# Kernel optimization log

Hardware: AMD Instinct MI355X
Metric: run time of the kernel (lower is better)

The kernel has to match this reference:

```python
import jax, jax.numpy as jnp
import numpy as np

HIDDEN = 1024
HEADS = 16
D_K = HIDDEN // HEADS
NEG_INF = -jnp.inf


def setup_inputs() -> dict:
    key = jax.random.key(0)
    ks = jax.random.split(key, 9)
    N, S = 4, 2048
    scale = 1.0 / np.sqrt(HIDDEN)
    x = jax.random.normal(ks[0], (N, S, HIDDEN), dtype=jnp.float32)
    attn_mask = jnp.ones((N, S), dtype=jnp.int32)
    Wq = jax.random.normal(ks[1], (HIDDEN, HIDDEN), dtype=jnp.float32) * scale
    bq = jnp.zeros((HIDDEN,), dtype=jnp.float32)
    Wk = jax.random.normal(ks[2], (HIDDEN, HIDDEN), dtype=jnp.float32) * scale
    bk = jnp.zeros((HIDDEN,), dtype=jnp.float32)
    Wv = jax.random.normal(ks[3], (HIDDEN, HIDDEN), dtype=jnp.float32) * scale
    bv = jnp.zeros((HIDDEN,), dtype=jnp.float32)
    Wp = jax.random.normal(ks[4], (HIDDEN, HIDDEN), dtype=jnp.float32) * scale
    bp = jnp.zeros((HIDDEN,), dtype=jnp.float32)
    return {"x": x, "attn_mask": attn_mask, "Wq": Wq, "bq": bq,
            "Wk": Wk, "bk": bk, "Wv": Wv, "bv": bv, "Wp": Wp, "bp": bp}


def reference(x, attn_mask, Wq, bq, Wk, bk, Wv, bv, Wp, bp):
    N, S, _ = x.shape
    H, dk = HEADS, D_K
    # torch nn.Linear: y = x @ W.T + b
    q = (x @ Wq.T + bq).reshape(N, S, H, dk).transpose(0, 2, 1, 3)  # (N,H,S,dk)
    k = (x @ Wk.T + bk).reshape(N, S, H, dk).transpose(0, 2, 1, 3)
    v = (x @ Wv.T + bv).reshape(N, S, H, dk).transpose(0, 2, 1, 3)
    attn = jnp.einsum('nhqd,nhkd->nhqk', q, k) / jnp.sqrt(jnp.float32(dk))
    mask = attn_mask.reshape(N, 1, 1, S)
    attn = jnp.where(mask == 0, NEG_INF, attn)
    attn = jax.nn.softmax(attn, axis=-1)
    # dropout is identity in eval mode
    y = jnp.einsum('nhqk,nhkd->nhqd', attn, v)  # (N,H,S,dk)
    y = y.transpose(0, 2, 1, 3).reshape(N, S, H * dk)
    return y @ Wp.T + bp
```

## Files before the change

### kernel.cpp

```cpp
#include <hip/hip_runtime.h>

typedef unsigned short u16;
typedef unsigned int u32;
typedef unsigned long long u64;
typedef __attribute__((ext_vector_type(8))) short bf16x8;
typedef __attribute__((ext_vector_type(4))) short bf16x4;
typedef __attribute__((ext_vector_type(4))) float f32x4;
typedef __attribute__((ext_vector_type(2))) unsigned int u32x2;

#define AS1(p) ((const __attribute__((address_space(1))) void*)(p))
#define AS3(p) ((__attribute__((address_space(3))) void*)(p))

__device__ __forceinline__ u16 f2bf(float f) {
    u32 u = __float_as_uint(f);
    u += 0x7fff + ((u >> 16) & 1);
    return (u16)(u >> 16);
}
__device__ __forceinline__ u32 pack2bf(float lo, float hi) {
    u32 a = __float_as_uint(lo) + 0x8000u;
    u32 b = __float_as_uint(hi) + 0x8000u;
    return __builtin_amdgcn_perm(b, a, 0x07060302);
}
__device__ __forceinline__ u32 cvtpk(float lo, float hi) {
    u32 r;
    asm("v_cvt_pk_bf16_f32 %0, %1, %2" : "=v"(r) : "v"(lo), "v"(hi));
    return r;
}

__device__ __forceinline__ void async16(const u16* g, u16* l) {
    __builtin_amdgcn_global_load_lds(AS1(g), AS3(l), 16, 0, 0);
}

__global__ __launch_bounds__(256) void cvt_kernel(const float* __restrict__ src,
                                                  u16* __restrict__ dst, int n) {
    int idx = (blockIdx.x * 256 + threadIdx.x) * 8;
    if (idx >= n) return;
    float4 a = *(const float4*)(src + idx);
    float4 b = *(const float4*)(src + idx + 4);
    uint4 o;
    o.x = (u32)f2bf(a.x) | ((u32)f2bf(a.y) << 16);
    o.y = (u32)f2bf(a.z) | ((u32)f2bf(a.w) << 16);
    o.z = (u32)f2bf(b.x) | ((u32)f2bf(b.y) << 16);
    o.w = (u32)f2bf(b.z) | ((u32)f2bf(b.w) << 16);
    *(uint4*)(dst + idx) = o;
}

__global__ __launch_bounds__(256) void cvt4_kernel(
    const float* __restrict__ s0, const float* __restrict__ s1,
    const float* __restrict__ s2, const float* __restrict__ s3,
    u16* __restrict__ d0, u16* __restrict__ d1,
    u16* __restrict__ d2, u16* __restrict__ d3) {
    const float* s; u16* d;
    switch (blockIdx.y) {
        case 0:  s = s0; d = d0; break;
        case 1:  s = s1; d = d1; break;
        case 2:  s = s2; d = d2; break;
        default: s = s3; d = d3; break;
    }
    int idx = (blockIdx.x * 256 + threadIdx.x) * 8;
    float4 a = *(const float4*)(s + idx);
    float4 b = *(const float4*)(s + idx + 4);
    uint4 o;
    o.x = (u32)f2bf(a.x) | ((u32)f2bf(a.y) << 16);
    o.y = (u32)f2bf(a.z) | ((u32)f2bf(a.w) << 16);
    o.z = (u32)f2bf(b.x) | ((u32)f2bf(b.y) << 16);
    o.w = (u32)f2bf(b.z) | ((u32)f2bf(b.w) << 16);
    *(uint4*)(d + idx) = o;
}

__global__ __launch_bounds__(256, 2) void gemm_bt(
    const u16* __restrict__ A,
    const u16* __restrict__ Wa, const u16* __restrict__ Wb, const u16* __restrict__ Wc,
    const float* __restrict__ ba, const float* __restrict__ bb, const float* __restrict__ bc,
    void* oa, void* ob_, void* oc, int mode)
{
    constexpr int K = 1024;
    __shared__ u16 smem[128 * 132];
    u16* At = smem;
    u16* Wt = smem + 4096;

    const int tid = threadIdx.x;
    const int lane = tid & 63, wv = tid >> 6;
    const int l15 = lane & 15, quad = lane >> 4;
    const int wr = wv >> 1, wc = wv & 1;

    const int L = blockIdx.x + (blockIdx.y << 3) + (blockIdx.z << 9);
    const int g = L & 7;
    const int j = L >> 3;
    const int z = j >> 6;
    const int r = j & 63;
    const int m0 = ((g << 3) + (r & 7)) * 128;
    const int n0 = (r >> 3) * 128;

    const u16* W = (z == 0) ? Wa : ((z == 1) ? Wb : Wc);
    const float* bs = (z == 0) ? ba : ((z == 1) ? bb : bc);
    void* out = (z == 0) ? oa : ((z == 1) ? ob_ : oc);
    const bool swap_ = (mode == 1) || (z < 2);

    f32x4 acc[4][4];
#pragma unroll
    for (int i = 0; i < 4; ++i)
#pragma unroll
        for (int j2 = 0; j2 < 4; ++j2) acc[i][j2] = (f32x4)0.f;

    const int call0 = wv * 2;
    for (int kk = 0; kk < K; kk += 32) {
#pragma unroll
        for (int jj = 0; jj < 2; ++jj) {
            int c = (call0 + jj) * 64 + lane;
            int row = c >> 2;
            int ko = ((c & 3) ^ (row & 3)) * 8;
            async16(A + (size_t)(m0 + row) * K + kk + ko, &At[(call0 + jj) * 512 + lane * 8]);
            async16(W + (size_t)(n0 + row) * K + kk + ko, &Wt[(call0 + jj) * 512 + lane * 8]);
        }
        __syncthreads();

        bf16x8 af[4], wf[4];
#pragma unroll
        for (int t = 0; t < 4; ++t) {
            int rowa = wr * 64 + t * 16 + l15;
            af[t] = *(const bf16x8*)&At[rowa * 32 + ((quad ^ (rowa & 3)) * 8)];
            int rowb = wc * 64 + t * 16 + l15;
            wf[t] = *(const bf16x8*)&Wt[rowb * 32 + ((quad ^ (rowb & 3)) * 8)];
        }
        if (swap_) {
#pragma unroll
            for (int rt = 0; rt < 4; ++rt)
#pragma unroll
                for (int ct = 0; ct < 4; ++ct)
                    acc[rt][ct] = __builtin_amdgcn_mfma_f32_16x16x32_bf16(wf[ct], af[rt], acc[rt][ct], 0, 0, 0);
        } else {
#pragma unroll
            for (int rt = 0; rt < 4; ++rt)
#pragma unroll
                for (int ct = 0; ct < 4; ++ct)
                    acc[rt][ct] = __builtin_amdgcn_mfma_f32_16x16x32_bf16(af[rt], wf[ct], acc[rt][ct], 0, 0, 0);
        }
        __syncthreads();
    }

    if (mode == 1) {
#pragma unroll
        for (int rt = 0; rt < 4; ++rt)
#pragma unroll
            for (int ct = 0; ct < 4; ++ct) {
                int m_ = m0 + wr * 64 + rt * 16 + l15;
                int ob = n0 + wc * 64 + ct * 16 + quad * 4;
                float4 b4 = *(const float4*)&bs[ob];
                float4 v;
                v.x = acc[rt][ct][0] + b4.x;
                v.y = acc[rt][ct][1] + b4.y;
                v.z = acc[rt][ct][2] + b4.z;
                v.w = acc[rt][ct][3] + b4.w;
                *(float4*)((float*)out + (size_t)m_ * 1024 + ob) = v;
            }
        return;
    }

    const int n = m0 >> 11, s0 = m0 & 2047;
    if (z < 2) {
        const float qs = (z == 0) ? 0.18033688011112042f : 1.0f;
#pragma unroll
        for (int rt = 0; rt < 4; ++rt)
#pragma unroll
            for (int ct = 0; ct < 4; ++ct) {
                int ml = wr * 64 + rt * 16 + l15;
                int ol = wc * 64 + ct * 16 + quad * 4;
                float4 b4 = *(const float4*)&bs[n0 + ol];
                float v0 = (acc[rt][ct][0] + b4.x) * qs;
                float v1 = (acc[rt][ct][1] + b4.y) * qs;
                float v2 = (acc[rt][ct][2] + b4.z) * qs;
                float v3 = (acc[rt][ct][3] + b4.w) * qs;
                u32x2 pv = { pack2bf(v0, v1), pack2bf(v2, v3) };
                *(u32x2*)&smem[ml * 132 + ol] = pv;
            }
        __syncthreads();
        const int h0 = n0 >> 6;
#pragma unroll
        for (int p = 0; p < 8; ++p) {
            int hh = p >> 2, qq = p & 3;
            int m = qq * 32 + (tid >> 3), d = (tid & 7) * 8;
            bf16x8 vv = *(const bf16x8*)&smem[m * 132 + hh * 64 + d];
            u16* dst = (u16*)out + ((size_t)((n * 16 + h0 + hh) * 2048 + s0 + m)) * 64 + d;
            *(bf16x8*)dst = vv;
        }
    } else {
#pragma unroll
        for (int rt = 0; rt < 4; ++rt)
#pragma unroll
            for (int ct = 0; ct < 4; ++ct) {
                int ol = wc * 64 + ct * 16 + l15;
                int ml = wr * 64 + rt * 16 + quad * 4;
                float b = bs[n0 + ol];
                float v0 = acc[rt][ct][0] + b;
                float v1 = acc[rt][ct][1] + b;
                float v2 = acc[rt][ct][2] + b;
                float v3 = acc[rt][ct][3] + b;
                u32x2 pv = { pack2bf(v0, v1), pack2bf(v2, v3) };
                *(u32x2*)&smem[ol * 132 + ml] = pv;
            }
        __syncthreads();
#pragma unroll
        for (int p = 0; p < 8; ++p) {
            int o = p * 16 + (tid >> 4), ms = (tid & 15) * 8;
            bf16x8 vv = *(const bf16x8*)&smem[o * 132 + ms];
            int og = n0 + o;
            int h = og >> 6, d = og & 63;
            u16* dst = (u16*)out + ((size_t)((n * 16 + h) * 64 + d)) * 2048 + s0 + ms;
            *(bf16x8*)dst = vv;
        }
    }
}

__global__ __launch_bounds__(256, 2) void attn_kernel(
    const u16* __restrict__ Q, const u16* __restrict__ K_,
    const u16* __restrict__ VT, const int* __restrict__ mask,
    u16* __restrict__ Y)
{
    constexpr int S = 2048, DK = 64, STR = 72;
    __shared__ u16 Kt[2][64 * STR];
    __shared__ u16 Vt[2][64 * STR];

    const int tid = threadIdx.x;
    const int lane = tid & 63, w = tid >> 6;
    const int l15 = lane & 15, quad = lane >> 4;

    const int L = blockIdx.x + (blockIdx.y << 3);
    const int vb = (L & 7) * 64 + (L >> 3);
    const int nh = vb >> 3;
    const int n = nh >> 4, h = nh & 15;
    const int qbase = (vb & 7) * 256;

    const u16* Qh = Q + (size_t)nh * S * DK;
    const u16* Kh = K_ + (size_t)nh * S * DK;
    const u16* Vh = VT + (size_t)nh * DK * S;

    bf16x8 qf[4][2];
#pragma unroll
    for (int nt = 0; nt < 4; ++nt)
#pragma unroll
        for (int st = 0; st < 2; ++st)
            qf[nt][st] = *(const bf16x8*)(Qh + (size_t)(qbase + w * 64 + nt * 16 + l15) * DK + st * 32 + quad * 8);

    f32x4 o[4][4];
#pragma unroll
    for (int dt = 0; dt < 4; ++dt)
#pragma unroll
        for (int nt = 0; nt < 4; ++nt) o[dt][nt] = (f32x4)0.f;
    float lsum[4] = {0.f, 0.f, 0.f, 0.f};

    const int r0 = tid >> 3, c8 = (tid & 7) * 8;

    u32 bm = 0;
    for (int t = 0; t < 32; ++t) {
        int mv = mask[n * S + t * 64 + lane];
        if (__ballot(mv != 0) == ~0ull) bm |= (1u << t);
    }

    {
        bf16x8 k0 = *(const bf16x8*)(Kh + (size_t)r0 * 64 + c8);
        bf16x8 k1 = *(const bf16x8*)(Kh + (size_t)(r0 + 32) * 64 + c8);
        bf16x8 v0 = *(const bf16x8*)(Vh + (size_t)r0 * S + c8);
        bf16x8 v1 = *(const bf16x8*)(Vh + (size_t)(r0 + 32) * S + c8);
        *(bf16x8*)&Kt[0][r0 * STR + c8] = k0;
        *(bf16x8*)&Kt[0][(r0 + 32) * STR + c8] = k1;
        *(bf16x8*)&Vt[0][r0 * STR + c8] = v0;
        *(bf16x8*)&Vt[0][(r0 + 32) * STR + c8] = v1;
    }
    __syncthreads();

    const f32x4 zf = (f32x4)0.f;

    for (int it = 0; it < 32; ++it) {
        const int cur = it & 1, nxt = cur ^ 1;
        const u16* Ktc = &Kt[cur][0];
        const u16* Vtc = &Vt[cur][0];

        const int kkn = ((it + 1) << 6) & (S - 1);
        bf16x8 rk0 = *(const bf16x8*)(Kh + (size_t)(kkn + r0) * 64 + c8);
        bf16x8 rk1 = *(const bf16x8*)(Kh + (size_t)(kkn + r0 + 32) * 64 + c8);
        bf16x8 rv0 = *(const bf16x8*)(Vh + (size_t)r0 * S + kkn + c8);
        bf16x8 rv1 = *(const bf16x8*)(Vh + (size_t)(r0 + 32) * S + kkn + c8);

        f32x4 sacc[4][4];
        __builtin_amdgcn_s_setprio(1);
#pragma unroll
        for (int jt = 0; jt < 4; ++jt) {
            bf16x8 kf = *(const bf16x8*)&Ktc[(jt * 16 + l15) * STR + quad * 8];
#pragma unroll
            for (int nt = 0; nt < 4; ++nt)
                sacc[jt][nt] = __builtin_amdgcn_mfma_f32_16x16x32_bf16(kf, qf[nt][0], zf, 0, 0, 0);
        }
#pragma unroll
        for (int jt = 0; jt < 4; ++jt) {
            bf16x8 kf = *(const bf16x8*)&Ktc[(jt * 16 + l15) * STR + 32 + quad * 8];
#pragma unroll
            for (int nt = 0; nt < 4; ++nt)
                sacc[jt][nt] = __builtin_amdgcn_mfma_f32_16x16x32_bf16(kf, qf[nt][1], sacc[jt][nt], 0, 0, 0);
        }
        __builtin_amdgcn_s_setprio(0);

        if (!((bm >> it) & 1)) {
#pragma unroll
            for (int jt = 0; jt < 4; ++jt)
#pragma unroll
                for (int r = 0; r < 4; ++r) {
                    int mv = mask[n * S + it * 64 + jt * 16 + quad * 4 + r];
#pragma unroll
                    for (int nt = 0; nt < 4; ++nt)
                        if (mv == 0) sacc[jt][nt][r] = -1e30f;
                }
        }

        bf16x8 pb[4][2];
#pragma unroll
        for (int nt = 0; nt < 4; ++nt) {
            float ps = 0.f;
            u32 pkx[4], pky[4];
#pragma unroll
            for (int jt = 0; jt < 4; ++jt) {
                float e0 = __builtin_amdgcn_exp2f(sacc[jt][nt][0]);
                float e1 = __builtin_amdgcn_exp2f(sacc[jt][nt][1]);
                float e2 = __builtin_amdgcn_exp2f(sacc[jt][nt][2]);
                float e3 = __builtin_amdgcn_exp2f(sacc[jt][nt][3]);
                ps += (e0 + e1) + (e2 + e3);
                pkx[jt] = cvtpk(e0, e1);
                pky[jt] = cvtpk(e2, e3);
            }
            lsum[nt] += ps;
#pragma unroll
            for (int kt = 0; kt < 2; ++kt) {
                auto rX = __builtin_amdgcn_permlane32_swap(pkx[2 * kt], pkx[2 * kt + 1], false, false);
                auto rY = __builtin_amdgcn_permlane32_swap(pky[2 * kt], pky[2 * kt + 1], false, false);
                auto sX = __builtin_amdgcn_permlane16_swap(rX[0], rX[1], false, false);
                auto sY = __builtin_amdgcn_permlane16_swap(rY[0], rY[1], false, false);
                union { u32 u[4]; bf16x8 v; } pu;
                pu.u[0] = sX[0];
                pu.u[1] = sY[0];
                pu.u[2] = sX[1];
                pu.u[3] = sY[1];
                pb[nt][kt] = pu.v;
            }
        }

        *(bf16x8*)&Kt[nxt][r0 * STR + c8] = rk0;
        *(bf16x8*)&Kt[nxt][(r0 + 32) * STR + c8] = rk1;
        *(bf16x8*)&Vt[nxt][r0 * STR + c8] = rv0;
        *(bf16x8*)&Vt[nxt][(r0 + 32) * STR + c8] = rv1;

        __builtin_amdgcn_s_setprio(1);
#pragma unroll
        for (int kt = 0; kt < 2; ++kt) {
#pragma unroll
            for (int dt = 0; dt < 4; ++dt) {
                bf16x8 vf = *(const bf16x8*)&Vtc[(dt * 16 + l15) * STR + kt * 32 + quad * 8];
#pragma unroll
                for (int nt = 0; nt < 4; ++nt)
                    o[dt][nt] = __builtin_amdgcn_mfma_f32_16x16x32_bf16(vf, pb[nt][kt], o[dt][nt], 0, 0, 0);
            }
        }
        __builtin_amdgcn_s_setprio(0);

        __syncthreads();
    }

#pragma unroll
    for (int nt = 0; nt < 4; ++nt) {
        float ls = lsum[nt];
        ls += __shfl_xor(ls, 16);
        ls += __shfl_xor(ls, 32);
        float rl = (ls > 0.f) ? 1.f / ls : 0.f;
        int qi = qbase + w * 64 + nt * 16 + l15;
#pragma unroll
        for (int dt = 0; dt < 4; ++dt) {
            u32x2 pv = { pack2bf(o[dt][nt][0] * rl, o[dt][nt][1] * rl),
                         pack2bf(o[dt][nt][2] * rl, o[dt][nt][3] * rl) };
            size_t base = ((size_t)(n * 2048 + qi)) * 1024 + h * 64 + dt * 16 + quad * 4;
            *(u32x2*)(Y + base) = pv;
        }
    }
}

extern "C" void kernel_launch(void* const* d_in, const int* in_sizes, int n_in,
                              void* d_out, int out_size, void* d_ws, size_t ws_size,
                              hipStream_t stream) {
    const float* x  = (const float*)d_in[0];
    const int* mask = (const int*)d_in[1];
    const float* Wq = (const float*)d_in[2];
    const float* bq = (const float*)d_in[3];
    const float* Wk = (const float*)d_in[4];
    const float* bk = (const float*)d_in[5];
    const float* Wv = (const float*)d_in[6];
    const float* bv = (const float*)d_in[7];
    const float* Wp = (const float*)d_in[8];
    const float* bp = (const float*)d_in[9];

    char* ws = (char*)d_ws;
    u16* xb  = (u16*)(ws);
    u16* wqb = (u16*)(ws + (16u << 20));
    u16* wkb = (u16*)(ws + (18u << 20));
    u16* wvb = (u16*)(ws + (20u << 20));
    u16* wpb = (u16*)(ws + (22u << 20));
    u16* Qb  = (u16*)(ws + (24u << 20));
    u16* Kb  = (u16*)(ws + (40u << 20));
    u16* Vb  = (u16*)(ws + (56u << 20));
    u16* Yb  = (u16*)(ws + (72u << 20));

    cvt_kernel<<<4096, 256, 0, stream>>>(x, xb, 8388608);
    cvt4_kernel<<<dim3(512, 4), 256, 0, stream>>>(Wq, Wk, Wv, Wp, wqb, wkb, wvb, wpb);

    gemm_bt<<<dim3(8, 64, 3), 256, 0, stream>>>(xb, wqb, wkb, wvb, bq, bk, bv,
                                                (void*)Qb, (void*)Kb, (void*)Vb, 0);

    attn_kernel<<<dim3(8, 64), 256, 0, stream>>>(Qb, Kb, Vb, mask, Yb);

    gemm_bt<<<dim3(8, 64, 1), 256, 0, stream>>>(Yb, wpb, wpb, wpb, bp, bp, bp,
                                                d_out, d_out, d_out, 1);
}
```

Before: 277.1 us.

## Software-pipeline attention loop so QK^T of next tile overlaps softmax/PV of previous

Restructures the flash-attention inner loop so that the QK^T MFMAs for tile t are interleaved with the exp2/pack softmax work of tile t-1, using two ping-pong score register sets (X/Yc) and a manually unrolled-by-two macro body. The prologue now preloads two K/V tiles and computes the first score tile up front. This is meant to hide transcendental and permlane latency behind matrix-core work. In exchange it raises register pressure, adds a second barrier per iteration and makes the tail handling (last body wraps around via the modulo index) more intricate.

```diff
diff --git a/kernel.cpp b/kernel.cpp
--- a/kernel.cpp
+++ b/kernel.cpp
@@ -257,112 +257,117 @@
         if (__ballot(mv != 0) == ~0ull) bm |= (1u << t);
     }
 
-    {
-        bf16x8 k0 = *(const bf16x8*)(Kh + (size_t)r0 * 64 + c8);
-        bf16x8 k1 = *(const bf16x8*)(Kh + (size_t)(r0 + 32) * 64 + c8);
-        bf16x8 v0 = *(const bf16x8*)(Vh + (size_t)r0 * S + c8);
-        bf16x8 v1 = *(const bf16x8*)(Vh + (size_t)(r0 + 32) * S + c8);
-        *(bf16x8*)&Kt[0][r0 * STR + c8] = k0;
-        *(bf16x8*)&Kt[0][(r0 + 32) * STR + c8] = k1;
-        *(bf16x8*)&Vt[0][r0 * STR + c8] = v0;
-        *(bf16x8*)&Vt[0][(r0 + 32) * STR + c8] = v1;
+#pragma unroll
+    for (int t = 0; t < 2; ++t) {
+        bf16x8 k0 = *(const bf16x8*)(Kh + (size_t)(t * 64 + r0) * 64 + c8);
+        bf16x8 k1 = *(const bf16x8*)(Kh + (size_t)(t * 64 + r0 + 32) * 64 + c8);
+        bf16x8 v0 = *(const bf16x8*)(Vh + (size_t)r0 * S + t * 64 + c8);
+        bf16x8 v1 = *(const bf16x8*)(Vh + (size_t)(r0 + 32) * S + t * 64 + c8);
+        *(bf16x8*)&Kt[t][r0 * STR + c8] = k0;
+        *(bf16x8*)&Kt[t][(r0 + 32) * STR + c8] = k1;
+        *(bf16x8*)&Vt[t][r0 * STR + c8] = v0;
+        *(bf16x8*)&Vt[t][(r0 + 32) * STR + c8] = v1;
     }
     __syncthreads();
 
     const f32x4 zf = (f32x4)0.f;
-
-    for (int it = 0; it < 32; ++it) {
-        const int cur = it & 1, nxt = cur ^ 1;
-        const u16* Ktc = &Kt[cur][0];
-        const u16* Vtc = &Vt[cur][0];
-
-        const int kkn = ((it + 1) << 6) & (S - 1);
-        bf16x8 rk0 = *(const bf16x8*)(Kh + (size_t)(kkn + r0) * 64 + c8);
-        bf16x8 rk1 = *(const bf16x8*)(Kh + (size_t)(kkn + r0 + 32) * 64 + c8);
-        bf16x8 rv0 = *(const bf16x8*)(Vh + (size_t)r0 * S + kkn + c8);
-        bf16x8 rv1 = *(const bf16x8*)(Vh + (size_t)(r0 + 32) * S + kkn + c8);
-
-        f32x4 sacc[4][4];
-        __builtin_amdgcn_s_setprio(1);
-#pragma unroll
-        for (int jt = 0; jt < 4; ++jt) {
-            bf16x8 kf = *(const bf16x8*)&Ktc[(jt * 16 + l15) * STR + quad * 8];
-#pragma unroll
-            for (int nt = 0; nt < 4; ++nt)
-                sacc[jt][nt] = __builtin_amdgcn_mfma_f32_16x16x32_bf16(kf, qf[nt][0], zf, 0, 0, 0);
-        }
-#pragma unroll
-        for (int jt = 0; jt < 4; ++jt) {
-            bf16x8 kf = *(const bf16x8*)&Ktc[(jt * 16 + l15) * STR + 32 + quad * 8];
-#pragma unroll
-            for (int nt = 0; nt < 4; ++nt)
-                sacc[jt][nt] = __builtin_amdgcn_mfma_f32_16x16x32_bf16(kf, qf[nt][1], sacc[jt][nt], 0, 0, 0);
-        }
-        __builtin_amdgcn_s_setprio(0);
-
-        if (!((bm >> it) & 1)) {
-#pragma unroll
-            for (int jt = 0; jt < 4; ++jt)
-#pragma unroll
-                for (int r = 0; r < 4; ++r) {
-                    int mv = mask[n * S + it * 64 + jt * 16 + quad * 4 + r];
-#pragma unroll
-                    for (int nt = 0; nt < 4; ++nt)
-                        if (mv == 0) sacc[jt][nt][r] = -1e30f;
-                }
-        }
-
-        bf16x8 pb[4][2];
+    f32x4 X[4][4], Yc[4][4];
+
+    __builtin_amdgcn_s_setprio(1);
+#pragma unroll
+    for (int jt = 0; jt < 4; ++jt) {
+        bf16x8 kf0 = *(const bf16x8*)&Kt[0][(jt * 16 + l15) * STR + quad * 8];
+        bf16x8 kf1 = *(const bf16x8*)&Kt[0][(jt * 16 + l15) * STR + 32 + quad * 8];
 #pragma unroll
         for (int nt = 0; nt < 4; ++nt) {
-            float ps = 0.f;
-            u32 pkx[4], pky[4];
-#pragma unroll
-            for (int jt = 0; jt < 4; ++jt) {
-                float e0 = __builtin_amdgcn_exp2f(sacc[jt][nt][0]);
-                float e1 = __builtin_amdgcn_exp2f(sacc[jt][nt][1]);
-                float e2 = __builtin_amdgcn_exp2f(sacc[jt][nt][2]);
-                float e3 = __builtin_amdgcn_exp2f(sacc[jt][nt][3]);
-                ps += (e0 + e1) + (e2 + e3);
-                pkx[jt] = cvtpk(e0, e1);
-                pky[jt] = cvtpk(e2, e3);
-            }
-            lsum[nt] += ps;
-#pragma unroll
-            for (int kt = 0; kt < 2; ++kt) {
-                auto rX = __builtin_amdgcn_permlane32_swap(pkx[2 * kt], pkx[2 * kt + 1], false, false);
-                auto rY = __builtin_amdgcn_permlane32_swap(pky[2 * kt], pky[2 * kt + 1], false, false);
-                auto sX = __builtin_amdgcn_permlane16_swap(rX[0], rX[1], false, false);
-                auto sY = __builtin_amdgcn_permlane16_swap(rY[0], rY[1], false, false);
-                union { u32 u[4]; bf16x8 v; } pu;
-                pu.u[0] = sX[0];
-                pu.u[1] = sY[0];
-                pu.u[2] = sX[1];
-                pu.u[3] = sY[1];
-                pb[nt][kt] = pu.v;
-            }
-        }
-
-        *(bf16x8*)&Kt[nxt][r0 * STR + c8] = rk0;
-        *(bf16x8*)&Kt[nxt][(r0 + 32) * STR + c8] = rk1;
-        *(bf16x8*)&Vt[nxt][r0 * STR + c8] = rv0;
-        *(bf16x8*)&Vt[nxt][(r0 + 32) * STR + c8] = rv1;
-
-        __builtin_amdgcn_s_setprio(1);
-#pragma unroll
-        for (int kt = 0; kt < 2; ++kt) {
-#pragma unroll
-            for (int dt = 0; dt < 4; ++dt) {
-                bf16x8 vf = *(const bf16x8*)&Vtc[(dt * 16 + l15) * STR + kt * 32 + quad * 8];
-#pragma unroll
-                for (int nt = 0; nt < 4; ++nt)
-                    o[dt][nt] = __builtin_amdgcn_mfma_f32_16x16x32_bf16(vf, pb[nt][kt], o[dt][nt], 0, 0, 0);
-            }
-        }
-        __builtin_amdgcn_s_setprio(0);
-
-        __syncthreads();
-    }
+            X[jt][nt] = __builtin_amdgcn_mfma_f32_16x16x32_bf16(kf0, qf[nt][0], zf, 0, 0, 0);
+            X[jt][nt] = __builtin_amdgcn_mfma_f32_16x16x32_bf16(kf1, qf[nt][1], X[jt][nt], 0, 0, 0);
+        }
+    }
+    __builtin_amdgcn_s_setprio(0);
+
+#define BODY(SP, SC, ITC) do {                                                           \
+    const int cur_ = (ITC) & 1, prv_ = cur_ ^ 1;                                         \
+    const int tm_ = (ITC) - 1;                                                           \
+    const int kkn_ = (((ITC) + 1) << 6) & (S - 1);                                       \
+    bf16x8 rk0_ = *(const bf16x8*)(Kh + (size_t)(kkn_ + r0) * 64 + c8);                  \
+    bf16x8 rk1_ = *(const bf16x8*)(Kh + (size_t)(kkn_ + r0 + 32) * 64 + c8);             \
+    if (!((bm >> tm_) & 1)) {                            \
+        for (int jt = 0; jt < 4; ++jt)                                                   \
+            for (int rr = 0; rr < 4; ++rr) {                                             \
+                int mv = mask[n * S + tm_ * 64 + jt * 16 + quad * 4 + rr];               \
+                for (int nt = 0; nt < 4; ++nt)                                           \
+                    if (mv == 0) SP[jt][nt][rr] = -1e30f;                                \
+            }                                                                            \
+    }                                                                                    \
+    u32 pkx_[4][4], pky_[4][4];                                            \
+    float ps_[4] = {0.f, 0.f, 0.f, 0.f};                                                 \
+    __builtin_amdgcn_s_setprio(1);                                                       \
+    _Pragma("unroll")                                                                    \
+    for (int jt = 0; jt < 4; ++jt) {                                                     \
+        bf16x8 kf0 = *(const bf16x8*)&Kt[cur_][(jt * 16 + l15) * STR + quad * 8];        \
+        bf16x8 kf1 = *(const bf16x8*)&Kt[cur_][(jt * 16 + l15) * STR + 32 + quad * 8];   \
+        _Pragma("unroll")                                                                \
+        for (int nt = 0; nt < 4; ++nt) {                                                 \
+            SC[jt][nt] = __builtin_amdgcn_mfma_f32_16x16x32_bf16(kf0, qf[nt][0], zf, 0, 0, 0); \
+            SC[jt][nt] = __builtin_amdgcn_mfma_f32_16x16x32_bf16(kf1, qf[nt][1], SC[jt][nt], 0, 0, 0); \
+        }                                                                                \
+        _Pragma("unroll")                                                                \
+        for (int nt = 0; nt < 4; ++nt) {          \
+            float e0 = __builtin_amdgcn_exp2f(SP[jt][nt][0]);                            \
+            float e1 = __builtin_amdgcn_exp2f(SP[jt][nt][1]);                            \
+            float e2 = __builtin_amdgcn_exp2f(SP[jt][nt][2]);                            \
+            float e3 = __builtin_amdgcn_exp2f(SP[jt][nt][3]);                            \
+            ps_[nt] += (e0 + e1) + (e2 + e3);                                            \
+            pkx_[nt][jt] = cvtpk(e0, e1);                                                \
+            pky_[nt][jt] = cvtpk(e2, e3);                                                \
+        }                                                                                \
+    }                                                                                    \
+    __builtin_amdgcn_s_setprio(0);                                                       \
+    bf16x8 pb_[4][2];                                                                    \
+    _Pragma("unroll")                                                                    \
+    for (int nt = 0; nt < 4; ++nt) {                                                     \
+        lsum[nt] += ps_[nt];                                                             \
+        _Pragma("unroll")                                                                \
+        for (int kt = 0; kt < 2; ++kt) {                                                 \
+            auto rX_ = __builtin_amdgcn_permlane32_swap(pkx_[nt][2 * kt], pkx_[nt][2 * kt + 1], false, false); \
+            auto rY_ = __builtin_amdgcn_permlane32_swap(pky_[nt][2 * kt], pky_[nt][2 * kt + 1], false, false); \
+            auto sX_ = __builtin_amdgcn_permlane16_swap(rX_[0], rX_[1], false, false);   \
+            auto sY_ = __builtin_amdgcn_permlane16_swap(rY_[0], rY_[1], false, false);   \
+            union { u32 u[4]; bf16x8 v; } pu_;                                           \
+            pu_.u[0] = sX_[0]; pu_.u[1] = sY_[0]; pu_.u[2] = sX_[1]; pu_.u[3] = sY_[1];  \
+            pb_[nt][kt] = pu_.v;                                                         \
+        }                                                                                \
+    }                                                                                    \
+    bf16x8 rv0_ = *(const bf16x8*)(Vh + (size_t)r0 * S + kkn_ + c8);                     \
+    bf16x8 rv1_ = *(const bf16x8*)(Vh + (size_t)(r0 + 32) * S + kkn_ + c8);              \
+    __builtin_amdgcn_s_setprio(1);                                                       \
+    _Pragma("unroll")                                                                    \
+    for (int kt = 0; kt < 2; ++kt) {                                                     \
+        _Pragma("unroll")                                                                \
+        for (int dt = 0; dt < 4; ++dt) {                                                 \
+            bf16x8 vf_ = *(const bf16x8*)&Vt[prv_][(dt * 16 + l15) * STR + kt * 32 + quad * 8]; \
+            _Pragma("unroll")                                                            \
+            for (int nt = 0; nt < 4; ++nt)                                               \
+                o[dt][nt] = __builtin_amdgcn_mfma_f32_16x16x32_bf16(vf_, pb_[nt][kt], o[dt][nt], 0, 0, 0); \
+        }                                                                                \
+    }                                                                                    \
+    __builtin_amdgcn_s_setprio(0);                                                       \
+    __syncthreads();        \
+    *(bf16x8*)&Kt[prv_][r0 * STR + c8] = rk0_;                                           \
+    *(bf16x8*)&Kt[prv_][(r0 + 32) * STR + c8] = rk1_;                                    \
+    *(bf16x8*)&Vt[prv_][r0 * STR + c8] = rv0_;                                           \
+    *(bf16x8*)&Vt[prv_][(r0 + 32) * STR + c8] = rv1_;                                    \
+    __syncthreads();                                             \
+} while (0)
+
+    for (int b = 1; b < 31; b += 2) {
+        BODY(X, Yc, b);
+        BODY(Yc, X, b + 1);
+    }
+    BODY(X, Yc, 31);
+    BODY(Yc, X, 32);
+#undef BODY
 
 #pragma unroll
     for (int nt = 0; nt < 4; ++nt) {
```

Result: slower. 427.8 us (+54.4%).

## Double-buffer GEMM LDS tiles to overlap async global loads with MFMA

Applied to the files above, without the earlier changes.

Splits the shared-memory staging area of the projection GEMM into two buffers, so the async global-to-LDS loads for the next K-slice are issued while MFMAs run on the current slice. Each step now needs one barrier instead of two, and the source and destination addresses are precomputed outside the loop. Nothing new is allocated, since the existing 128x132 shared array already covers both buffers. The risks are a race if the waitcnt and barrier placement is wrong (waitcnt only covers the issuing thread's loads), and added register pressure under the 2-blocks-per-CU launch bound.

```diff
diff --git a/kernel.cpp b/kernel.cpp
--- a/kernel.cpp
+++ b/kernel.cpp
@@ -76,8 +76,6 @@
 {
     constexpr int K = 1024;
     __shared__ u16 smem[128 * 132];
-    u16* At = smem;
-    u16* Wt = smem + 4096;
 
     const int tid = threadIdx.x;
     const int lane = tid & 63, wv = tid >> 6;
@@ -103,25 +101,34 @@
 #pragma unroll
         for (int j2 = 0; j2 < 4; ++j2) acc[i][j2] = (f32x4)0.f;
 
-    const int call0 = wv * 2;
-    for (int kk = 0; kk < K; kk += 32) {
-#pragma unroll
-        for (int jj = 0; jj < 2; ++jj) {
-            int c = (call0 + jj) * 64 + lane;
-            int row = c >> 2;
-            int ko = ((c & 3) ^ (row & 3)) * 8;
-            async16(A + (size_t)(m0 + row) * K + kk + ko, &At[(call0 + jj) * 512 + lane * 8]);
-            async16(W + (size_t)(n0 + row) * K + kk + ko, &Wt[(call0 + jj) * 512 + lane * 8]);
-        }
-        __syncthreads();
-
+    const int c0 = (wv * 2) * 64 + lane;
+    const int c1 = c0 + 64;
+    const int row0 = c0 >> 2, row1 = c1 >> 2;
+    const int ko0 = ((c0 & 3) ^ (row0 & 3)) * 8;
+    const int ko1 = ((c1 & 3) ^ (row1 & 3)) * 8;
+    const u16* As0 = A + (size_t)(m0 + row0) * K + ko0;
+    const u16* As1 = A + (size_t)(m0 + row1) * K + ko1;
+    const u16* Ws0 = W + (size_t)(n0 + row0) * K + ko0;
+    const u16* Ws1 = W + (size_t)(n0 + row1) * K + ko1;
+    const int off0 = c0 * 8, off1 = c1 * 8;
+
+    u16* const At0 = smem;         u16* const Wt0 = smem + 4096;
+    u16* const At1 = smem + 8192;  u16* const Wt1 = smem + 12288;
+
+    auto stage = [&](u16* Atb, u16* Wtb, int kk) {
+        async16(As0 + kk, Atb + off0);
+        async16(As1 + kk, Atb + off1);
+        async16(Ws0 + kk, Wtb + off0);
+        async16(Ws1 + kk, Wtb + off1);
+    };
+    auto compute = [&](const u16* Atb, const u16* Wtb) {
         bf16x8 af[4], wf[4];
 #pragma unroll
         for (int t = 0; t < 4; ++t) {
             int rowa = wr * 64 + t * 16 + l15;
-            af[t] = *(const bf16x8*)&At[rowa * 32 + ((quad ^ (rowa & 3)) * 8)];
+            af[t] = *(const bf16x8*)&Atb[rowa * 32 + ((quad ^ (rowa & 3)) * 8)];
             int rowb = wc * 64 + t * 16 + l15;
-            wf[t] = *(const bf16x8*)&Wt[rowb * 32 + ((quad ^ (rowb & 3)) * 8)];
+            wf[t] = *(const bf16x8*)&Wtb[rowb * 32 + ((quad ^ (rowb & 3)) * 8)];
         }
         if (swap_) {
 #pragma unroll
@@ -136,8 +143,28 @@
                 for (int ct = 0; ct < 4; ++ct)
                     acc[rt][ct] = __builtin_amdgcn_mfma_f32_16x16x32_bf16(af[rt], wf[ct], acc[rt][ct], 0, 0, 0);
         }
-        __syncthreads();
-    }
+    };
+
+    stage(At0, Wt0, 0);
+    asm volatile("s_waitcnt vmcnt(0)" ::: "memory");
+    __builtin_amdgcn_s_barrier();
+
+#pragma unroll 1
+    for (int kk = 0; kk < K - 64; kk += 64) {
+        stage(At1, Wt1, kk + 32);
+        compute(At0, Wt0);
+        asm volatile("s_waitcnt vmcnt(0)" ::: "memory");
+        __builtin_amdgcn_s_barrier();
+        stage(At0, Wt0, kk + 64);
+        compute(At1, Wt1);
+        asm volatile("s_waitcnt vmcnt(0)" ::: "memory");
+        __builtin_amdgcn_s_barrier();
+    }
+    stage(At1, Wt1, 992);
+    compute(At0, Wt0);
+    asm volatile("s_waitcnt vmcnt(0)" ::: "memory");
+    __builtin_amdgcn_s_barrier();
+    compute(At1, Wt1);
 
     if (mode == 1) {
 #pragma unroll
@@ -156,6 +183,8 @@
             }
         return;
     }
+
+    __syncthreads();
 
     const int n = m0 >> 11, s0 = m0 & 2047;
     if (z < 2) {
```

Result: faster. 268.7 us (-3.0%).

## Triple-buffer GEMM K-loop with async loads and MFMA priority boost

Applied to the files above, without the earlier changes.

Replaces the single-buffered GEMM K-loop, which synchronized twice per 32-wide K step, with a three-stage shared-memory ring. Tile loads are issued two steps ahead and synchronized with a partial vmcnt wait and one barrier per step. Global addresses are hoisted out of the loop, and s_setprio raises wave priority around the MFMA block. Shared memory grows to 48KB per block, which may limit occupancy, and a barrier is added before the epilogue reuses that memory.

```diff
diff --git a/kernel.cpp b/kernel.cpp
--- a/kernel.cpp
+++ b/kernel.cpp
@@ -75,9 +75,7 @@
     void* oa, void* ob_, void* oc, int mode)
 {
     constexpr int K = 1024;
-    __shared__ u16 smem[128 * 132];
-    u16* At = smem;
-    u16* Wt = smem + 4096;
+    __shared__ u16 smem[24576];
 
     const int tid = threadIdx.x;
     const int lane = tid & 63, wv = tid >> 6;
@@ -103,18 +101,28 @@
 #pragma unroll
         for (int j2 = 0; j2 < 4; ++j2) acc[i][j2] = (f32x4)0.f;
 
-    const int call0 = wv * 2;
-    for (int kk = 0; kk < K; kk += 32) {
-#pragma unroll
-        for (int jj = 0; jj < 2; ++jj) {
-            int c = (call0 + jj) * 64 + lane;
-            int row = c >> 2;
-            int ko = ((c & 3) ^ (row & 3)) * 8;
-            async16(A + (size_t)(m0 + row) * K + kk + ko, &At[(call0 + jj) * 512 + lane * 8]);
-            async16(W + (size_t)(n0 + row) * K + kk + ko, &Wt[(call0 + jj) * 512 + lane * 8]);
-        }
-        __syncthreads();
-
+    const int c0 = (wv * 2) * 64 + lane;
+    const int c1 = c0 + 64;
+    const int row0 = c0 >> 2, row1 = c1 >> 2;
+    const int ko0 = ((c0 & 3) ^ (row0 & 3)) * 8;
+    const int ko1 = ((c1 & 3) ^ (row1 & 3)) * 8;
+    const u16* As0 = A + (size_t)(m0 + row0) * K + ko0;
+    const u16* As1 = A + (size_t)(m0 + row1) * K + ko1;
+    const u16* Ws0 = W + (size_t)(n0 + row0) * K + ko0;
+    const u16* Ws1 = W + (size_t)(n0 + row1) * K + ko1;
+    const int off0 = c0 * 8, off1 = c1 * 8;
+
+    auto stage = [&](int buf, int kk) {
+        u16* At = smem + buf * 8192;
+        u16* Wt = At + 4096;
+        async16(As0 + kk, At + off0);
+        async16(As1 + kk, At + off1);
+        async16(Ws0 + kk, Wt + off0);
+        async16(Ws1 + kk, Wt + off1);
+    };
+    auto compute = [&](int buf) {
+        const u16* At = smem + buf * 8192;
+        const u16* Wt = At + 4096;
         bf16x8 af[4], wf[4];
 #pragma unroll
         for (int t = 0; t < 4; ++t) {
@@ -123,6 +131,7 @@
             int rowb = wc * 64 + t * 16 + l15;
             wf[t] = *(const bf16x8*)&Wt[rowb * 32 + ((quad ^ (rowb & 3)) * 8)];
         }
+        __builtin_amdgcn_s_setprio(1);
         if (swap_) {
 #pragma unroll
             for (int rt = 0; rt < 4; ++rt)
@@ -136,8 +145,26 @@
                 for (int ct = 0; ct < 4; ++ct)
                     acc[rt][ct] = __builtin_amdgcn_mfma_f32_16x16x32_bf16(af[rt], wf[ct], acc[rt][ct], 0, 0, 0);
         }
-        __syncthreads();
-    }
+        __builtin_amdgcn_s_setprio(0);
+    };
+
+#define W4 asm volatile("s_waitcnt vmcnt(4)" ::: "memory")
+#define W0 asm volatile("s_waitcnt vmcnt(0)" ::: "memory")
+#define BAR __builtin_amdgcn_s_barrier()
+
+    stage(0, 0);
+    stage(1, 32);
+#pragma unroll 1
+    for (int kk = 64; kk < 1024; kk += 96) {
+        W4; BAR; stage(2, kk);      compute(0);
+        W4; BAR; stage(0, kk + 32); compute(1);
+        W4; BAR; stage(1, kk + 64); compute(2);
+    }
+    W4; BAR; compute(0);
+    W0; BAR; compute(1);
+#undef W4
+#undef W0
+#undef BAR
 
     if (mode == 1) {
 #pragma unroll
@@ -156,6 +183,8 @@
             }
         return;
     }
+
+    __syncthreads();
 
     const int n = m0 >> 11, s0 = m0 & 2047;
     if (z < 2) {
```

New measurement: 264.7 us. 4.5% less time.
